# Performance work log

Measured on AMD Instinct MI355X. Metric: run time of the kernel, lower is better.

## Reference

```python
import jax, jax.numpy as jnp
import numpy as np


def setup_inputs() -> dict:
    key = jax.random.key(0)
    pred = jax.random.normal(key, (16, 4, 768, 768), dtype=jnp.float32)
    return {"pred": pred}


def _largest_cc(mask):
    """Largest 4-connected component of a 2D boolean mask, as float32 0/1.

    Equivalent to scipy.ndimage.label (default 4-connectivity) followed by
    keeping the largest label. Uses min-label flood propagation: each
    foreground pixel starts with its raster index; iterated neighbor-min
    converges so every pixel holds its component's minimum pixel index
    (the 'root'). Ties in size resolve to the smallest root, which matches
    scipy's label-order tie-breaking (labels assigned in raster order).
    """
    H, W = mask.shape
    HW = H * W
    idx = jnp.arange(HW, dtype=jnp.int32).reshape(H, W)
    BIG = jnp.int32(HW)  # sentinel for background
    lbl0 = jnp.where(mask, idx, BIG)

    def body(carry):
        lbl, _ = carry
        p = jnp.pad(lbl, 1, constant_values=HW)
        nb = jnp.minimum(jnp.minimum(p[:-2, 1:-1], p[2:, 1:-1]),
                         jnp.minimum(p[1:-1, :-2], p[1:-1, 2:]))
        new = jnp.where(mask, jnp.minimum(lbl, nb), BIG)
        return new, jnp.any(new != lbl)

    lbl, _ = jax.lax.while_loop(lambda c: c[1], body, (lbl0, jnp.any(mask)))

    # component sizes keyed by root pixel index; background bucket = HW
    sizes = jax.ops.segment_sum(mask.ravel().astype(jnp.int32), lbl.ravel(),
                                num_segments=HW + 1)
    sizes = sizes.at[HW].set(0)
    root = jnp.argmax(sizes).astype(jnp.int32)
    return ((lbl == root) & mask).astype(jnp.float32)


def reference(pred):
    B, C, H, W = pred.shape
    labels = jnp.argmax(pred, axis=1)  # [B, H, W]
    cls = jnp.arange(1, C, dtype=labels.dtype)
    masks = labels[:, None, :, :] == cls[None, :, None, None]  # [B, C-1, H, W]
    comp = jax.vmap(_largest_cc)(masks.reshape(-1, H, W)).reshape(B, C - 1, H, W)
    bg = 1.0 - jnp.clip(comp.sum(axis=1), 0.0, 1.0)  # channel 0
    return jnp.concatenate([bg[:, None], comp], axis=1)
```

## Files before the change

### kernel.cpp

```cpp
#include <hip/hip_runtime.h>
#include <stdint.h>

#define BB 16
#define CC 4
#define HH 768
#define WW 768
#define HW (HH * WW)
#define NPIX (BB * HW)
#define NIMG (BB * (CC - 1))
#define BEST_STRIDE 16

#define TS 64
#define TPI (WW / TS)
#define TILES_PER_IMG (TPI * TPI)
#define TPIX (TS * TS)
#define CCL_TPB 256

typedef unsigned long long ull;


__device__ __forceinline__ int find_root(int* P, int i) {
    int p = P[i];
    while (p != i) {
        int gp = P[p];
        P[i] = gp;
        i = p;
        p = gp;
    }
    return i;
}

__device__ __forceinline__ void merge(int* P, int a, int b) {
    a = find_root(P, a);
    b = find_root(P, b);
    while (a != b) {
        if (a < b) { int t = a; a = b; b = t; }
        int old = atomicCAS(&P[a], a, b);
        if (old == a) return;
        a = find_root(P, old);
        b = find_root(P, b);
    }
}


__device__ __forceinline__ int lfind(int* P, int i) {
    int p = P[i];
    while (p != i) {
        int gp = P[p];
        P[i] = gp;
        i = p;
        p = gp;
    }
    return i;
}

__device__ __forceinline__ void lmerge(int* P, int a, int b) {
    a = lfind(P, a);
    b = lfind(P, b);
    while (a != b) {
        if (a < b) { int t = a; a = b; b = t; }
        int old = atomicCAS(&P[a], a, b);
        if (old == a) return;
        a = lfind(P, old);
        b = lfind(P, b);
    }
}

__device__ __forceinline__ int lfind_masked(int* P, int i) {
    int p = P[i] & 0xFFFF;
    while (p != i) {
        int gp = P[p] & 0xFFFF;
        P[i] = gp;
        i = p;
        p = gp;
    }
    return i;
}

__device__ __forceinline__ ull umax64(ull a, ull b) { return a > b ? a : b; }


__global__ __launch_bounds__(CCL_TPB) void k_tile_ccl(
        const float* __restrict__ pred,
        uint8_t* __restrict__ labels,
        int* __restrict__ parent,
        uint32_t* __restrict__ counts,
        ull* __restrict__ best) {
    __shared__ int sp[TPIX];
    __shared__ uint8_t slab[TPIX];

    if (blockIdx.x == 0) {
        for (int i = threadIdx.x; i < NIMG * BEST_STRIDE; i += CCL_TPB) best[i] = 0ull;
    }

    const int tid = (int)threadIdx.x;
    const int img = blockIdx.x / TILES_PER_IMG;
    const int tile = blockIdx.x % TILES_PER_IMG;
    const int tr = (tile / TPI) * TS;
    const int tc = (tile % TPI) * TS;
    const float* pb = pred + (size_t)img * CC * HW;
    const int imgbase = img * HW;

    for (int k = 0; k < TPIX; k += CCL_TPB * 4) {
        int li = k + tid * 4;
        int gi = (tr + (li >> 6)) * WW + tc + (li & 63);
        float4 v0 = *(const float4*)&pb[gi];
        float4 v1 = *(const float4*)&pb[gi + HW];
        float4 v2 = *(const float4*)&pb[gi + 2 * HW];
        float4 v3 = *(const float4*)&pb[gi + 3 * HW];
        const float* a0 = &v0.x; const float* a1 = &v1.x;
        const float* a2 = &v2.x; const float* a3 = &v3.x;
        uchar4 lout;
        uint8_t* lj = &lout.x;
        #pragma unroll
        for (int j = 0; j < 4; ++j) {
            int lab = 0;
            float bv = a0[j];
            if (a1[j] > bv) { bv = a1[j]; lab = 1; }
            if (a2[j] > bv) { bv = a2[j]; lab = 2; }
            if (a3[j] > bv) { bv = a3[j]; lab = 3; }
            lj[j] = (uint8_t)lab;
        }
        *(uchar4*)&slab[li] = lout;
        *(uchar4*)&labels[imgbase + gi] = lout;
    }
    __syncthreads();

    const int c = tid & 63;

    #pragma unroll 1
    for (int it = 0; it < TPIX / CCL_TPB; ++it) {
        int li = it * CCL_TPB + tid;
        int lab = slab[li];
        int labL = __shfl_up(lab, 1, 64);
        bool isStart = lab && (c == 0 || labL != lab);
        ull mask = __ballot(isStart);
        int v = -1;
        if (lab) {
            ull mle = mask & (~0ull >> (63 - c));
            v = (li & ~63) + (63 - __clzll(mle));
        }
        sp[li] = v;
    }
    __syncthreads();

    #pragma unroll 1
    for (int it = 0; it < TPIX / CCL_TPB; ++it) {
        int li = it * CCL_TPB + tid;
        int lab = slab[li];
        int labU = (li >= TS) ? (int)slab[li - TS] : 0;
        int labL = __shfl_up(lab, 1, 64);
        int labUL = __shfl_up(labU, 1, 64);
        if (lab && labU == lab) {
            if (c == 0 || !(labL == lab && labUL == lab))
                lmerge(sp, li, li - TS);
        }
    }
    __syncthreads();

    #pragma unroll 1
    for (int it = 0; it < TPIX / CCL_TPB; ++it) {
        int li = it * CCL_TPB + tid;
        int gidx = imgbase + (tr + (li >> 6)) * WW + tc + (li & 63);
        int s0 = sp[li];
        int pv = -1;
        uint8_t flag = 0;
        if (s0 >= 0) {
            int root = lfind_masked(sp, li);
            atomicAdd((unsigned int*)&sp[root], 0x10000u);
            flag = (uint8_t)(root == li);
            pv = imgbase + (tr + (root >> 6)) * WW + tc + (root & 63);
        }
        slab[li] = flag;
        parent[gidx] = pv;
    }
    __syncthreads();

    for (int k = 0; k < TPIX; k += CCL_TPB * 4) {
        int li = k + tid * 4;
        int gi = imgbase + (tr + (li >> 6)) * WW + tc + (li & 63);
        uchar4 fl = *(const uchar4*)&slab[li];
        int4 sv = *(const int4*)&sp[li];
        uint4 cout;
        cout.x = fl.x ? ((uint32_t)sv.x >> 16) : 0u;
        cout.y = fl.y ? ((uint32_t)sv.y >> 16) : 0u;
        cout.z = fl.z ? ((uint32_t)sv.z >> 16) : 0u;
        cout.w = fl.w ? ((uint32_t)sv.w >> 16) : 0u;
        *(uint4*)&counts[gi] = cout;
    }
}

#define VEDGES ((TPI - 1) * HH)
#define EDGES_PER_IMG (2 * (TPI - 1) * HH)
__global__ void k_border_merge(const uint8_t* __restrict__ labels, int* parent) {
    int t = blockIdx.x * blockDim.x + threadIdx.x;
    if (t >= BB * EDGES_PER_IMG) return;
    int img = t / EDGES_PER_IMG;
    int e = t % EDGES_PER_IMG;
    int a, b;
    if (e < VEDGES) {
        int j = e / HH, r = e % HH;
        int c = j * TS + TS - 1;
        a = r * WW + c;
        b = a + 1;
    } else {
        e -= VEDGES;
        int j = e / WW, c = e % WW;
        int r = j * TS + TS - 1;
        a = r * WW + c;
        b = a + WW;
    }
    int ga = img * HW + a, gb = img * HW + b;
    uint8_t la = labels[ga];
    if (la && labels[gb] == la) merge(parent, ga, gb);
}

__global__ void k_compress(int* __restrict__ parent, uint32_t* __restrict__ counts) {
    int t = blockIdx.x * blockDim.x + threadIdx.x;
    if (t >= NPIX) return;
    uint32_t cnt = counts[t];
    if (!cnt) return;
    int g = parent[t];
    if (g == t) return;
    while (true) { int pg = parent[g]; if (pg == g) break; g = pg; }
    parent[t] = g;
    atomicAdd(&counts[g], cnt);
    counts[t] = 0;
}

#define BEST_BLK_PER_IMG 144
#define BEST_TPB 256
#define BEST_PIX_PER_BLK (HW / BEST_BLK_PER_IMG)
__global__ void k_best(const uint8_t* __restrict__ labels,
                       const uint32_t* __restrict__ counts,
                       ull* __restrict__ best) {
    __shared__ ull sw[(BEST_TPB / 64) * 3];
    int img = blockIdx.x / BEST_BLK_PER_IMG;
    int chunk = blockIdx.x % BEST_BLK_PER_IMG;
    int base = img * HW + chunk * BEST_PIX_PER_BLK;

    ull l0 = 0, l1 = 0, l2 = 0;
    for (int k = 0; k < BEST_PIX_PER_BLK; k += BEST_TPB * 4) {
        int t = base + k + (int)threadIdx.x * 4;
        uint4 cv = *(const uint4*)&counts[t];
        if (cv.x | cv.y | cv.z | cv.w) {
            uchar4 lv = *(const uchar4*)&labels[t];
            uint32_t cs[4] = {cv.x, cv.y, cv.z, cv.w};
            uint8_t ls[4] = {lv.x, lv.y, lv.z, lv.w};
            #pragma unroll
            for (int j = 0; j < 4; ++j) {
                if (cs[j]) {
                    int cc = (int)ls[j] - 1;
                    ull key = ((ull)cs[j] << 32) | (ull)(~(uint32_t)(t + j));
                    if (cc == 0) l0 = umax64(l0, key);
                    else if (cc == 1) l1 = umax64(l1, key);
                    else l2 = umax64(l2, key);
                }
            }
        }
    }
    #pragma unroll
    for (int m = 1; m < 64; m <<= 1) {
        l0 = umax64(l0, __shfl_xor(l0, m, 64));
        l1 = umax64(l1, __shfl_xor(l1, m, 64));
        l2 = umax64(l2, __shfl_xor(l2, m, 64));
    }
    int lane = threadIdx.x & 63;
    int wid = threadIdx.x >> 6;
    if (lane == 0) { sw[wid * 3 + 0] = l0; sw[wid * 3 + 1] = l1; sw[wid * 3 + 2] = l2; }
    __syncthreads();
    if (threadIdx.x < 3) {
        ull m = 0;
        for (int w = 0; w < BEST_TPB / 64; ++w) m = umax64(m, sw[w * 3 + threadIdx.x]);
        if (m) atomicMax(&best[(img * 3 + (int)threadIdx.x) * BEST_STRIDE], m);
    }
}

__global__ void k_output(const uint8_t* __restrict__ labels,
                         const int* __restrict__ parent,
                         const ull* __restrict__ best,
                         float* __restrict__ out) {
    int q = blockIdx.x * blockDim.x + threadIdx.x;
    if (q >= NPIX / 4) return;
    int t = q * 4;
    int b = t / HW;
    int i = t - b * HW;
    uchar4 lv = *(const uchar4*)&labels[t];
    int4 pv = *(const int4*)&parent[t];
    int root[3];
    root[0] = (int)(~(uint32_t)best[(b * 3 + 0) * BEST_STRIDE]);
    root[1] = (int)(~(uint32_t)best[(b * 3 + 1) * BEST_STRIDE]);
    root[2] = (int)(~(uint32_t)best[(b * 3 + 2) * BEST_STRIDE]);

    uint8_t ls[4] = {lv.x, lv.y, lv.z, lv.w};
    int ps[4] = {pv.x, pv.y, pv.z, pv.w};
    float fg[4];
    #pragma unroll
    for (int j = 0; j < 4; ++j) {
        int g = -1;
        if (ps[j] >= 0) g = parent[ps[j]];
        fg[j] = (ls[j] && g == root[ls[j] - 1]) ? 1.0f : 0.0f;
    }

    float4 o0, o1, o2, o3;
    float* c0 = &o0.x; float* c1 = &o1.x; float* c2 = &o2.x; float* c3 = &o3.x;
    #pragma unroll
    for (int j = 0; j < 4; ++j) {
        c0[j] = 1.0f - fg[j];
        c1[j] = (ls[j] == 1) ? fg[j] : 0.0f;
        c2[j] = (ls[j] == 2) ? fg[j] : 0.0f;
        c3[j] = (ls[j] == 3) ? fg[j] : 0.0f;
    }
    float* o = out + (size_t)b * CC * HW + i;
    *(float4*)&o[0] = o0;
    *(float4*)&o[HW] = o1;
    *(float4*)&o[2 * HW] = o2;
    *(float4*)&o[3 * HW] = o3;
}


extern "C" void kernel_launch(void* const* d_in, const int* in_sizes, int n_in,
                              void* d_out, int out_size, void* d_ws, size_t ws_size,
                              hipStream_t stream) {
    const float* pred = (const float*)d_in[0];
    float* out = (float*)d_out;

    uint8_t* labels = (uint8_t*)d_ws;
    int* parent = (int*)((char*)d_ws + NPIX);
    ull* best = (ull*)((char*)d_ws + NPIX + (size_t)NPIX * 4);
    uint32_t* counts = (uint32_t*)d_out;

    const int TPB = 256;

    k_tile_ccl<<<BB * TILES_PER_IMG, CCL_TPB, 0, stream>>>(pred, labels, parent, counts, best);
    k_border_merge<<<(BB * EDGES_PER_IMG + TPB - 1) / TPB, TPB, 0, stream>>>(labels, parent);
    k_compress<<<(NPIX + TPB - 1) / TPB, TPB, 0, stream>>>(parent, counts);
    k_best<<<BB * BEST_BLK_PER_IMG, BEST_TPB, 0, stream>>>(labels, counts, best);
    k_output<<<(NPIX / 4 + TPB - 1) / TPB, TPB, 0, stream>>>(labels, parent, best, out);
}
```

Baseline: 152.0 us.

## Flatten tile union-find by pointer jumping and count component sizes per run

```diff
diff --git a/kernel.cpp b/kernel.cpp
--- a/kernel.cpp
+++ b/kernel.cpp
@@ -66,17 +66,6 @@
     }
 }
 
-__device__ __forceinline__ int lfind_masked(int* P, int i) {
-    int p = P[i] & 0xFFFF;
-    while (p != i) {
-        int gp = P[p] & 0xFFFF;
-        P[i] = gp;
-        i = p;
-        p = gp;
-    }
-    return i;
-}
-
 __device__ __forceinline__ ull umax64(ull a, ull b) { return a > b ? a : b; }
 
 
@@ -86,8 +75,9 @@
         int* __restrict__ parent,
         uint32_t* __restrict__ counts,
         ull* __restrict__ best) {
-    __shared__ int sp[TPIX];
-    __shared__ uint8_t slab[TPIX];
+    __shared__ __align__(16) int sp[TPIX];
+    __shared__ __align__(16) uint8_t slab[TPIX];
+    __shared__ int changed;
 
     if (blockIdx.x == 0) {
         for (int i = threadIdx.x; i < NIMG * BEST_STRIDE; i += CCL_TPB) best[i] = 0ull;
@@ -135,7 +125,7 @@
         int labL = __shfl_up(lab, 1, 64);
         bool isStart = lab && (c == 0 || labL != lab);
         ull mask = __ballot(isStart);
-        int v = -1;
+        int v = li;
         if (lab) {
             ull mle = mask & (~0ull >> (63 - c));
             v = (li & ~63) + (63 - __clzll(mle));
@@ -158,34 +148,63 @@
     }
     __syncthreads();
 
+    for (;;) {
+        if (tid == 0) changed = 0;
+        __syncthreads();
+        int any = 0;
+        #pragma unroll 1
+        for (int it = 0; it < TPIX / CCL_TPB; ++it) {
+            int li = it * CCL_TPB + tid;
+            int v = sp[li];
+            int w = sp[v];
+            if (w != v) { sp[li] = w; any = 1; }
+        }
+        if (any) changed = 1;
+        __syncthreads();
+        int go = changed;
+        __syncthreads();
+        if (!go) break;
+    }
+
     #pragma unroll 1
     for (int it = 0; it < TPIX / CCL_TPB; ++it) {
         int li = it * CCL_TPB + tid;
-        int gidx = imgbase + (tr + (li >> 6)) * WW + tc + (li & 63);
-        int s0 = sp[li];
-        int pv = -1;
-        uint8_t flag = 0;
-        if (s0 >= 0) {
-            int root = lfind_masked(sp, li);
-            atomicAdd((unsigned int*)&sp[root], 0x10000u);
-            flag = (uint8_t)(root == li);
-            pv = imgbase + (tr + (root >> 6)) * WW + tc + (root & 63);
-        }
-        slab[li] = flag;
-        parent[gidx] = pv;
+        int lab = slab[li];
+        int labL = __shfl_up(lab, 1, 64);
+        bool isStart = lab && (c == 0 || labL != lab);
+        bool isEnd = lab && (c == 63 || (int)slab[li + 1] != lab);
+        ull endmask = __ballot(isEnd);
+        if (isStart) {
+            ull mge = endmask & (~0ull << c);
+            int epos = __ffsll((long long)mge) - 1;
+            int runlen = epos - c + 1;
+            int root = sp[li] & 0xFFFF;
+            atomicAdd((unsigned int*)&sp[root], (unsigned int)runlen << 16);
+        }
     }
     __syncthreads();
 
     for (int k = 0; k < TPIX; k += CCL_TPB * 4) {
         int li = k + tid * 4;
         int gi = imgbase + (tr + (li >> 6)) * WW + tc + (li & 63);
-        uchar4 fl = *(const uchar4*)&slab[li];
+        uchar4 lv = *(const uchar4*)&slab[li];
         int4 sv = *(const int4*)&sp[li];
-        uint4 cout;
-        cout.x = fl.x ? ((uint32_t)sv.x >> 16) : 0u;
-        cout.y = fl.y ? ((uint32_t)sv.y >> 16) : 0u;
-        cout.z = fl.z ? ((uint32_t)sv.z >> 16) : 0u;
-        cout.w = fl.w ? ((uint32_t)sv.w >> 16) : 0u;
+        const uint8_t* lj = &lv.x;
+        const int* sj = &sv.x;
+        int4 pout; uint4 cout;
+        int* pj = &pout.x; uint32_t* cj = &cout.x;
+        #pragma unroll
+        for (int j = 0; j < 4; ++j) {
+            int root = sj[j] & 0xFFFF;
+            if (lj[j]) {
+                pj[j] = imgbase + (tr + (root >> 6)) * WW + tc + (root & 63);
+                cj[j] = (root == li + j) ? ((uint32_t)sj[j] >> 16) : 0u;
+            } else {
+                pj[j] = -1;
+                cj[j] = 0u;
+            }
+        }
+        *(int4*)&parent[gi] = pout;
         *(uint4*)&counts[gi] = cout;
     }
 }
```

Measured after the change: 155.3 us. +2.2%, slower.
